# Optimization experiments

Measured on AMD Instinct MI355X. Metric: run time of the kernel, lower is better.

Reference implementation:

```python
import jax, jax.numpy as jnp
import numpy as np

N, M, B = 1024, 8192, 8192  # W: [N, M], x: [B, N]
BLOCK = 32


def activation_quant(x):
    # per-tensor symmetric int8 fake-quant with STE
    scale = 127.0 / jnp.clip(jnp.max(jnp.abs(x)), 1e-8, None)
    x_q = jnp.clip(jnp.round(x * scale), -128.0, 127.0) / scale
    return x + jax.lax.stop_gradient(x_q - x)


def weight_quant_q2_k(w, block_size=BLOCK):
    # blockwise 2-bit quant with top-2 outliers kept at 4-bit, STE
    shape = w.shape
    wf = w.reshape(-1)
    n = wf.shape[0]
    pad = (-n) % block_size
    wf = jnp.pad(wf, (0, pad))
    blocks = wf.reshape(-1, block_size)
    scales = jnp.clip(jnp.max(jnp.abs(blocks), axis=1, keepdims=True), 1e-8, None)
    nb = blocks / scales
    k = min(2, block_size)
    _, top_idx = jax.lax.top_k(jnp.abs(nb), k)
    rows = jnp.arange(nb.shape[0])[:, None]
    top_mask = jnp.zeros(nb.shape, dtype=bool).at[rows, top_idx].set(True)
    q4 = jnp.round(nb * 7.0) / 7.0
    abs_nb = jnp.abs(nb)
    q2 = jnp.sign(nb) * jnp.where(abs_nb > 0.66, 1.0, 1.0 / 3.0)
    q = jnp.where(top_mask, q4, q2) * scales
    w_q = q.reshape(-1)[:n].reshape(shape)
    return w + jax.lax.stop_gradient(w_q - w)


def setup_inputs() -> dict:
    key = jax.random.key(0)
    k1, k2, k3 = jax.random.split(key, 3)
    x = jax.random.normal(k1, (B, N), dtype=jnp.float32)
    W = jax.random.normal(k2, (N, M), dtype=jnp.float32) / np.float32(np.sqrt(M))
    b = jax.random.normal(k3, (N,), dtype=jnp.float32)
    idx = jnp.arange(M // 2, dtype=jnp.int32)            # expanded (quantized) columns
    idx_comp = jnp.arange(M // 2, M, dtype=jnp.int32)    # continuous columns
    return {"x": x, "W": W, "b": b, "idx": idx, "idx_comp": idx_comp}


def reference(x, W, b, idx, idx_comp):
    W_exp_q = weight_quant_q2_k(jnp.take(W, idx, axis=1))   # [N, M/2]
    W_cont = jnp.take(W, idx_comp, axis=1)                  # [N, M/2]
    hidden_exp = activation_quant(x) @ W_exp_q              # [B, M/2]
    hidden_cont = x @ W_cont                                # [B, M/2]
    hidden = (jnp.zeros((x.shape[0], M), dtype=x.dtype)
              .at[:, idx].set(hidden_exp)
              .at[:, idx_comp].set(hidden_cont))            # scatter back to [B, M]
    h_exp = activation_quant(hidden[:, idx])
    out = jax.nn.relu(h_exp @ W_exp_q.T + hidden[:, idx_comp] @ W_cont.T + b)
    return out
```

## Files before the change

kernel.cpp:

```cpp
#include <hip/hip_runtime.h>
#include <hip/hip_bf16.h>
#include <cstdint>


using bf16x8 = __attribute__((ext_vector_type(8))) __bf16;
using f32x4  = __attribute__((ext_vector_type(4))) float;

typedef const __attribute__((address_space(1))) void g_void;
typedef __attribute__((address_space(3))) void l_void;

__device__ __forceinline__ void gload16(const void* g, void* l) {
  __builtin_amdgcn_global_load_lds((g_void*)g, (l_void*)l, 16, 0, 0);
}

__device__ __forceinline__ ushort f2bf(float f) {
  union { float f; unsigned u; } c; c.f = f;
  unsigned r = c.u + 0x7FFFu + ((c.u >> 16) & 1u);
  return (ushort)(r >> 16);
}
__device__ __forceinline__ float bf2f(ushort u) {
  union { unsigned u; float f; } c; c.u = ((unsigned)u) << 16;
  return c.f;
}

__global__ void prep_wa_kernel(const float* __restrict__ W,
                               const float4* __restrict__ x,
                               ushort* __restrict__ Wq,
                               ushort* __restrict__ Wcb,
                               unsigned* __restrict__ amax_bits) {
  const int bidx = blockIdx.x;
  const int tid = threadIdx.x;

  if (bidx < 16384) {
    const int lane = tid & 63;
    const int wave = tid >> 6;
    const int e = lane & 31;
    const int half = lane >> 5;
    const int qb = bidx * 8 + wave * 2 + half;
    const int row = qb >> 7;
    const int m0 = (qb & 127) * 32;
    const float w = W[(size_t)row * 8192 + m0 + e];
    float aw = fabsf(w);
    float m = aw;
    #pragma unroll
    for (int d = 1; d <= 16; d <<= 1) m = fmaxf(m, __shfl_xor(m, d));
    int idx = (aw == m) ? e : 32;
    #pragma unroll
    for (int d = 1; d <= 16; d <<= 1) idx = min(idx, __shfl_xor(idx, d));
    const int i1 = idx;
    float a2 = (e == i1) ? -1.f : aw;
    float m2 = a2;
    #pragma unroll
    for (int d = 1; d <= 16; d <<= 1) m2 = fmaxf(m2, __shfl_xor(m2, d));
    int idx2 = (a2 == m2) ? e : 32;
    #pragma unroll
    for (int d = 1; d <= 16; d <<= 1) idx2 = min(idx2, __shfl_xor(idx2, d));
    const int i2 = idx2;

    const float scale = fmaxf(m, 1e-8f);
    const float nb = w / scale;
    float q;
    if (e == i1 || e == i2) {
      q = rintf(nb * 7.f) / 7.f;
    } else {
      float s = (nb > 0.f) ? 1.f : ((nb < 0.f) ? -1.f : 0.f);
      q = s * ((fabsf(nb) > 0.66f) ? 1.f : (1.f / 3.f));
    }
    Wq[(size_t)row * 4096 + m0 + e] = f2bf(q * scale);
  } else if (bidx < 20480) {
    const int u = (bidx - 16384) * 256 + tid;
    const int row = u >> 10;
    const int c4 = u & 1023;
    float4 v = *(const float4*)(W + (size_t)row * 8192 + 4096 + c4 * 4);
    ushort4 o;
    o.x = f2bf(v.x); o.y = f2bf(v.y); o.z = f2bf(v.z); o.w = f2bf(v.w);
    *(ushort4*)(Wcb + (size_t)row * 4096 + c4 * 4) = o;
  } else {
    float m = 0.f;
    const int base = (bidx - 20480) * 256 + tid;
    const int stride = 2048 * 256;
    for (int i = base; i < 8192 * 1024 / 4; i += stride) {
      float4 v = x[i];
      m = fmaxf(m, fmaxf(fmaxf(fabsf(v.x), fabsf(v.y)),
                         fmaxf(fabsf(v.z), fabsf(v.w))));
    }
    #pragma unroll
    for (int off = 32; off > 0; off >>= 1) m = fmaxf(m, __shfl_down(m, off));
    __shared__ float wm[4];
    int lane = tid & 63, wave = tid >> 6;
    if (lane == 0) wm[wave] = m;
    __syncthreads();
    if (tid == 0) {
      float r = fmaxf(fmaxf(wm[0], wm[1]), fmaxf(wm[2], wm[3]));
      atomicMax(amax_bits, __float_as_uint(r));
    }
  }
}

__global__ void prep_xt_kernel(const ushort* __restrict__ Wq,
                               ushort* __restrict__ WqT,
                               const float4* __restrict__ x,
                               const unsigned* __restrict__ amax_bits,
                               uint4* __restrict__ xq, uint4* __restrict__ xbf) {
  const int bidx = blockIdx.x;
  const int tid = threadIdx.x;

  if (bidx < 1024) {
    __shared__ ushort tile[64][68];
    const int ct = bidx & 63;
    const int rt = bidx >> 6;
    const int col0 = ct * 64, row0 = rt * 64;
    #pragma unroll
    for (int it = 0; it < 4; ++it) {
      const int r = (tid >> 4) + it * 16;
      const int c4 = (tid & 15) * 4;
      *(ushort4*)&tile[r][c4] =
          *(const ushort4*)(Wq + (size_t)(row0 + r) * 4096 + col0 + c4);
    }
    __syncthreads();
    #pragma unroll
    for (int it = 0; it < 4; ++it) {
      const int c = tid >> 2;
      const int rc = (tid & 3) + it * 4;
      ushort4 o;
      o.x = tile[rc * 4 + 0][c];
      o.y = tile[rc * 4 + 1][c];
      o.z = tile[rc * 4 + 2][c];
      o.w = tile[rc * 4 + 3][c];
      *(ushort4*)(WqT + (size_t)(col0 + c) * 1024 + row0 + rc * 4) = o;
    }
  } else {
    const float amax = fmaxf(__uint_as_float(*amax_bits), 1e-8f);
    const float scale = 127.f / amax;
    const int base = (bidx - 1024) * 256 + tid;
    const int stride = 2048 * 256;
    const int n8 = 8192 * 1024 / 8;
    for (int i = base; i < n8; i += stride) {
      float4 a = x[i * 2], b = x[i * 2 + 1];
      float v[8] = {a.x, a.y, a.z, a.w, b.x, b.y, b.z, b.w};
      unsigned qw[4], bw[4];
      #pragma unroll
      for (int j = 0; j < 4; ++j) {
        float q0 = fminf(fmaxf(rintf(v[2 * j] * scale), -128.f), 127.f) / scale;
        float q1 = fminf(fmaxf(rintf(v[2 * j + 1] * scale), -128.f), 127.f) / scale;
        qw[j] = (unsigned)f2bf(q0) | ((unsigned)f2bf(q1) << 16);
        bw[j] = (unsigned)f2bf(v[2 * j]) | ((unsigned)f2bf(v[2 * j + 1]) << 16);
      }
      xq[i] = make_uint4(qw[0], qw[1], qw[2], qw[3]);
      xbf[i] = make_uint4(bw[0], bw[1], bw[2], bw[3]);
    }
  }
}

__global__ __launch_bounds__(256, 2) void gemm1_kernel(
    const ushort* __restrict__ Wcb,
    ushort* __restrict__ G,
    const ushort* __restrict__ Aq, const ushort* __restrict__ BT,
    ushort* __restrict__ Hexp, unsigned* __restrict__ amax_bits) {
  __shared__ __align__(16) ushort As[2][128 * 32];
  __shared__ __align__(16) ushort Bs[2][128 * 32];
  __shared__ float wredmax[4];

  const int bidx = blockIdx.x;
  const int tid = threadIdx.x;
  const int lane = tid & 63, wave = tid >> 6;
  const int l15 = lane & 15, quad = lane >> 4;

  if (bidx < 256) {
    const int gy = bidx >> 4, gx = bidx & 15;
    const int i0 = gy * 64, j0 = gx * 64;
    const int wm2 = (wave >> 1) << 5, wn2 = (wave & 1) << 5;

    const ushort* Ag = Wcb + (size_t)(i0 + (tid >> 2)) * 4096 + (tid & 3) * 8;
    const ushort* Bg = Wcb + (size_t)(j0 + (tid >> 2)) * 4096 + (tid & 3) * 8;
    ushort* Asl = (ushort*)As;
    ushort* Bsl = (ushort*)Bs;

    f32x4 acc[2][2];
    #pragma unroll
    for (int i = 0; i < 2; ++i)
      #pragma unroll
      for (int j = 0; j < 2; ++j) acc[i][j] = (f32x4){0.f, 0.f, 0.f, 0.f};

    for (int k0 = 0; k0 < 4096; k0 += 64) {
      __syncthreads();
      gload16(Ag + k0, Asl + tid * 8);
      gload16(Bg + k0, Bsl + tid * 8);
      gload16(Ag + k0 + 32, Asl + 2048 + tid * 8);
      gload16(Bg + k0 + 32, Bsl + 2048 + tid * 8);
      __syncthreads();
      #pragma unroll
      for (int p = 0; p < 2; ++p) {
        bf16x8 af[2], bfr[2];
        #pragma unroll
        for (int i = 0; i < 2; ++i)
          af[i] = *(const bf16x8*)&Asl[p * 2048 + (wm2 + i * 16 + l15) * 32 + quad * 8];
        #pragma unroll
        for (int j = 0; j < 2; ++j)
          bfr[j] = *(const bf16x8*)&Bsl[p * 2048 + (wn2 + j * 16 + l15) * 32 + quad * 8];
        #pragma unroll
        for (int i = 0; i < 2; ++i)
          #pragma unroll
          for (int j = 0; j < 2; ++j)
            acc[i][j] = __builtin_amdgcn_mfma_f32_16x16x32_bf16(af[i], bfr[j], acc[i][j], 0, 0, 0);
      }
    }
    const int row0 = i0 + wm2 + quad * 4;
    const int col0 = j0 + wn2 + l15;
    #pragma unroll
    for (int i = 0; i < 2; ++i)
      #pragma unroll
      for (int j = 0; j < 2; ++j)
        #pragma unroll
        for (int r = 0; r < 4; ++r)
          G[(size_t)(row0 + i * 16 + r) * 1024 + (col0 + j * 16)] = f2bf(acc[i][j][r]);
    return;
  }

  const int l = bidx - 256;
  const int xcd = l & 7;
  const int s = l >> 3;
  const int t = (xcd << 2) | (s >> 6);
  const int u = s & 63;
  const int bx = ((t & 3) << 3) | (u & 7);
  const int by = ((t >> 2) << 3) | (u >> 3);

  const int wm = (wave >> 1) << 6, wn = (wave & 1) << 6;

  const ushort* Ag = Aq + (size_t)(by * 128 + (tid >> 2)) * 1024 + (tid & 3) * 8;
  const ushort* Bg = BT + (size_t)(bx * 128 + (tid >> 2)) * 1024 + (tid & 3) * 8;
  ushort* Asl0 = As[0] + tid * 8; ushort* Asl1 = As[1] + tid * 8;
  ushort* Bsl0 = Bs[0] + tid * 8; ushort* Bsl1 = Bs[1] + tid * 8;

  f32x4 acc[4][4];
  #pragma unroll
  for (int i = 0; i < 4; ++i)
    #pragma unroll
    for (int j = 0; j < 4; ++j) acc[i][j] = (f32x4){0.f, 0.f, 0.f, 0.f};

  for (int k0 = 0; k0 < 1024; k0 += 64) {
    __syncthreads();
    gload16(Ag + k0, Asl0);
    gload16(Ag + 64 * 1024 + k0, Asl0 + 64 * 32);
    gload16(Bg + k0, Bsl0);
    gload16(Bg + 64 * 1024 + k0, Bsl0 + 64 * 32);
    gload16(Ag + k0 + 32, Asl1);
    gload16(Ag + 64 * 1024 + k0 + 32, Asl1 + 64 * 32);
    gload16(Bg + k0 + 32, Bsl1);
    gload16(Bg + 64 * 1024 + k0 + 32, Bsl1 + 64 * 32);
    __syncthreads();

    #pragma unroll
    for (int p = 0; p < 2; ++p) {
      bf16x8 af[4], bfr[4];
      #pragma unroll
      for (int i = 0; i < 4; ++i)
        af[i] = *(const bf16x8*)&As[p][(wm + i * 16 + l15) * 32 + quad * 8];
      #pragma unroll
      for (int j = 0; j < 4; ++j)
        bfr[j] = *(const bf16x8*)&Bs[p][(wn + j * 16 + l15) * 32 + quad * 8];
      #pragma unroll
      for (int i = 0; i < 4; ++i)
        #pragma unroll
        for (int j = 0; j < 4; ++j)
          acc[i][j] = __builtin_amdgcn_mfma_f32_16x16x32_bf16(af[i], bfr[j], acc[i][j], 0, 0, 0);
    }
  }

  const int row0 = by * 128 + wm + quad * 4;
  const int col0 = bx * 128 + wn + l15;
  float lmax = 0.f;
  #pragma unroll
  for (int i = 0; i < 4; ++i)
    #pragma unroll
    for (int j = 0; j < 4; ++j)
      #pragma unroll
      for (int r = 0; r < 4; ++r) {
        float v = acc[i][j][r];
        lmax = fmaxf(lmax, fabsf(v));
        Hexp[(size_t)(row0 + i * 16 + r) * 4096 + (col0 + j * 16)] = f2bf(v);
      }

  #pragma unroll
  for (int off = 32; off > 0; off >>= 1)
    lmax = fmaxf(lmax, __shfl_down(lmax, off));
  if (lane == 0) wredmax[wave] = lmax;
  __syncthreads();
  if (tid == 0) {
    float m = fmaxf(fmaxf(wredmax[0], wredmax[1]), fmaxf(wredmax[2], wredmax[3]));
    atomicMax(amax_bits, __float_as_uint(m));
  }
}

__global__ void quant_h_kernel(ushort* __restrict__ H,
                               const unsigned* __restrict__ amax_bits) {
  const float amax = fmaxf(__uint_as_float(*amax_bits), 1e-8f);
  const float scale = 127.f / amax;
  const int n8 = 8192 * 4096 / 8;
  for (int i = blockIdx.x * blockDim.x + threadIdx.x; i < n8;
       i += gridDim.x * blockDim.x) {
    uint4* p = (uint4*)H + i;
    uint4 a = *p;
    unsigned w[4] = {a.x, a.y, a.z, a.w};
    #pragma unroll
    for (int j = 0; j < 4; ++j) {
      float lo = bf2f((ushort)(w[j] & 0xFFFF));
      float hi = bf2f((ushort)(w[j] >> 16));
      lo = fminf(fmaxf(rintf(lo * scale), -128.f), 127.f) / scale;
      hi = fminf(fmaxf(rintf(hi * scale), -128.f), 127.f) / scale;
      w[j] = (unsigned)f2bf(lo) | ((unsigned)f2bf(hi) << 16);
    }
    *p = make_uint4(w[0], w[1], w[2], w[3]);
  }
}

__global__ __launch_bounds__(256, 2) void gemm2_kernel(
    const ushort* __restrict__ Hq, const ushort* __restrict__ Wq,
    const ushort* __restrict__ Xb, const ushort* __restrict__ G,
    const float* __restrict__ bias, float* __restrict__ out) {
  __shared__ __align__(16) ushort As[2][128 * 32];
  __shared__ __align__(16) ushort Bs[2][128 * 32];

  const int l = blockIdx.x;
  const int xcd = l & 7;
  const int s = l >> 3;
  const int by = (xcd << 3) | (s >> 3);
  const int bx = s & 7;

  const int tid = threadIdx.x;
  const int lane = tid & 63, wave = tid >> 6;
  const int wm = (wave >> 1) << 6, wn = (wave & 1) << 6;
  const int l15 = lane & 15, quad = lane >> 4;

  ushort* Asl0 = As[0] + tid * 8; ushort* Asl1 = As[1] + tid * 8;
  ushort* Bsl0 = Bs[0] + tid * 8; ushort* Bsl1 = Bs[1] + tid * 8;

  f32x4 acc[4][4];
  #pragma unroll
  for (int i = 0; i < 4; ++i)
    #pragma unroll
    for (int j = 0; j < 4; ++j) acc[i][j] = (f32x4){0.f, 0.f, 0.f, 0.f};

  {
    const ushort* Ag = Hq + (size_t)(by * 128 + (tid >> 2)) * 4096 + (tid & 3) * 8;
    const ushort* Bg = Wq + (size_t)(bx * 128 + (tid >> 2)) * 4096 + (tid & 3) * 8;
    for (int k0 = 0; k0 < 4096; k0 += 64) {
      __syncthreads();
      gload16(Ag + k0, Asl0);
      gload16(Ag + (size_t)64 * 4096 + k0, Asl0 + 64 * 32);
      gload16(Bg + k0, Bsl0);
      gload16(Bg + (size_t)64 * 4096 + k0, Bsl0 + 64 * 32);
      gload16(Ag + k0 + 32, Asl1);
      gload16(Ag + (size_t)64 * 4096 + k0 + 32, Asl1 + 64 * 32);
      gload16(Bg + k0 + 32, Bsl1);
      gload16(Bg + (size_t)64 * 4096 + k0 + 32, Bsl1 + 64 * 32);
      __syncthreads();
      #pragma unroll
      for (int p = 0; p < 2; ++p) {
        bf16x8 af[4], bfr[4];
        #pragma unroll
        for (int i = 0; i < 4; ++i)
          af[i] = *(const bf16x8*)&As[p][(wm + i * 16 + l15) * 32 + quad * 8];
        #pragma unroll
        for (int j = 0; j < 4; ++j)
          bfr[j] = *(const bf16x8*)&Bs[p][(wn + j * 16 + l15) * 32 + quad * 8];
        #pragma unroll
        for (int i = 0; i < 4; ++i)
          #pragma unroll
          for (int j = 0; j < 4; ++j)
            acc[i][j] = __builtin_amdgcn_mfma_f32_16x16x32_bf16(af[i], bfr[j], acc[i][j], 0, 0, 0);
      }
    }
  }
  {
    const ushort* Ag = Xb + (size_t)(by * 128 + (tid >> 2)) * 1024 + (tid & 3) * 8;
    const ushort* Bg = G + (size_t)(bx * 128 + (tid >> 2)) * 1024 + (tid & 3) * 8;
    for (int k0 = 0; k0 < 1024; k0 += 64) {
      __syncthreads();
      gload16(Ag + k0, Asl0);
      gload16(Ag + 64 * 1024 + k0, Asl0 + 64 * 32);
      gload16(Bg + k0, Bsl0);
      gload16(Bg + 64 * 1024 + k0, Bsl0 + 64 * 32);
      gload16(Ag + k0 + 32, Asl1);
      gload16(Ag + 64 * 1024 + k0 + 32, Asl1 + 64 * 32);
      gload16(Bg + k0 + 32, Bsl1);
      gload16(Bg + 64 * 1024 + k0 + 32, Bsl1 + 64 * 32);
      __syncthreads();
      #pragma unroll
      for (int p = 0; p < 2; ++p) {
        bf16x8 af[4], bfr[4];
        #pragma unroll
        for (int i = 0; i < 4; ++i)
          af[i] = *(const bf16x8*)&As[p][(wm + i * 16 + l15) * 32 + quad * 8];
        #pragma unroll
        for (int j = 0; j < 4; ++j)
          bfr[j] = *(const bf16x8*)&Bs[p][(wn + j * 16 + l15) * 32 + quad * 8];
        #pragma unroll
        for (int i = 0; i < 4; ++i)
          #pragma unroll
          for (int j = 0; j < 4; ++j)
            acc[i][j] = __builtin_amdgcn_mfma_f32_16x16x32_bf16(af[i], bfr[j], acc[i][j], 0, 0, 0);
      }
    }
  }

  const int row0 = by * 128 + wm + quad * 4;
  const int col0 = bx * 128 + wn + l15;
  #pragma unroll
  for (int i = 0; i < 4; ++i)
    #pragma unroll
    for (int j = 0; j < 4; ++j) {
      float bv = bias[col0 + j * 16];
      #pragma unroll
      for (int r = 0; r < 4; ++r) {
        float v = acc[i][j][r] + bv;
        v = fmaxf(v, 0.f);
        out[(size_t)(row0 + i * 16 + r) * 1024 + (col0 + j * 16)] = v;
      }
    }
}

extern "C" void kernel_launch(void* const* d_in, const int* in_sizes, int n_in,
                              void* d_out, int out_size, void* d_ws, size_t ws_size,
                              hipStream_t stream) {
  (void)in_sizes; (void)n_in; (void)out_size; (void)ws_size;
  const float* x = (const float*)d_in[0];
  const float* W = (const float*)d_in[1];
  const float* b = (const float*)d_in[2];

  char* ws = (char*)d_ws;
  unsigned* scal = (unsigned*)ws;
  ushort* xq   = (ushort*)(ws + 256);
  ushort* xbf  = xq   + (size_t)8192 * 1024;
  ushort* Wq   = xbf  + (size_t)8192 * 1024;
  ushort* WqT  = Wq   + (size_t)1024 * 4096;
  ushort* Wcb  = WqT  + (size_t)4096 * 1024;
  ushort* G    = Wcb  + (size_t)1024 * 4096;
  ushort* Hexp = G    + (size_t)1024 * 1024;

  hipMemsetAsync(scal, 0, 256, stream);
  prep_wa_kernel<<<22528, 256, 0, stream>>>(W, (const float4*)x, Wq, Wcb, scal);
  prep_xt_kernel<<<3072, 256, 0, stream>>>(Wq, WqT, (const float4*)x, scal,
                                           (uint4*)xq, (uint4*)xbf);
  gemm1_kernel<<<2304, 256, 0, stream>>>(Wcb, G, xq, WqT, Hexp, scal + 1);
  quant_h_kernel<<<2048, 256, 0, stream>>>(Hexp, scal + 1);
  gemm2_kernel<<<512, 256, 0, stream>>>(Hexp, Wq, xbf, G, b, (float*)d_out);
}
```

Baseline: 358.3 us.

## Fuse weight transpose into quantization and enlarge Gram GEMM tiles

Writes the transposed quantized weight directly from the quantization pass via an LDS tile, removing a separate transpose pass that re-read Wq. The Gram GEMM on the continuous weights now uses 128x128 tiles (64 blocks) instead of 64x64 (256 blocks), improving reuse but making fewer, longer blocks that may form a tail. The quant_h launch grid is also doubled.

```diff
diff --git a/kernel.cpp b/kernel.cpp
--- a/kernel.cpp
+++ b/kernel.cpp
@@ -26,49 +26,64 @@
 __global__ void prep_wa_kernel(const float* __restrict__ W,
                                const float4* __restrict__ x,
                                ushort* __restrict__ Wq,
+                               ushort* __restrict__ WqT,
                                ushort* __restrict__ Wcb,
                                unsigned* __restrict__ amax_bits) {
   const int bidx = blockIdx.x;
   const int tid = threadIdx.x;
 
-  if (bidx < 16384) {
-    const int lane = tid & 63;
-    const int wave = tid >> 6;
-    const int e = lane & 31;
-    const int half = lane >> 5;
-    const int qb = bidx * 8 + wave * 2 + half;
-    const int row = qb >> 7;
-    const int m0 = (qb & 127) * 32;
-    const float w = W[(size_t)row * 8192 + m0 + e];
-    float aw = fabsf(w);
-    float m = aw;
-    #pragma unroll
-    for (int d = 1; d <= 16; d <<= 1) m = fmaxf(m, __shfl_xor(m, d));
-    int idx = (aw == m) ? e : 32;
-    #pragma unroll
-    for (int d = 1; d <= 16; d <<= 1) idx = min(idx, __shfl_xor(idx, d));
-    const int i1 = idx;
-    float a2 = (e == i1) ? -1.f : aw;
-    float m2 = a2;
-    #pragma unroll
-    for (int d = 1; d <= 16; d <<= 1) m2 = fmaxf(m2, __shfl_xor(m2, d));
-    int idx2 = (a2 == m2) ? e : 32;
-    #pragma unroll
-    for (int d = 1; d <= 16; d <<= 1) idx2 = min(idx2, __shfl_xor(idx2, d));
-    const int i2 = idx2;
-
-    const float scale = fmaxf(m, 1e-8f);
-    const float nb = w / scale;
-    float q;
-    if (e == i1 || e == i2) {
-      q = rintf(nb * 7.f) / 7.f;
-    } else {
-      float s = (nb > 0.f) ? 1.f : ((nb < 0.f) ? -1.f : 0.f);
-      q = s * ((fabsf(nb) > 0.66f) ? 1.f : (1.f / 3.f));
-    }
-    Wq[(size_t)row * 4096 + m0 + e] = f2bf(q * scale);
-  } else if (bidx < 20480) {
-    const int u = (bidx - 16384) * 256 + tid;
+  if (bidx < 1024) {
+    __shared__ __align__(16) ushort tile[64][72];
+    const int rt = bidx >> 6;
+    const int ct = bidx & 63;
+    const int r0 = rt * 64, c0 = ct * 64;
+    const int e = tid & 31;
+    const int hw = tid >> 5;
+    #pragma unroll
+    for (int it = 0; it < 16; ++it) {
+      const int g = it * 8 + hw;
+      const int row = g >> 1;
+      const int cg = (g & 1) * 32;
+      const float w = W[(size_t)(r0 + row) * 8192 + c0 + cg + e];
+      float aw = fabsf(w);
+      float m = aw;
+      #pragma unroll
+      for (int d = 1; d <= 16; d <<= 1) m = fmaxf(m, __shfl_xor(m, d));
+      int idx = (aw == m) ? e : 32;
+      #pragma unroll
+      for (int d = 1; d <= 16; d <<= 1) idx = min(idx, __shfl_xor(idx, d));
+      const int i1 = idx;
+      float a2 = (e == i1) ? -1.f : aw;
+      float m2 = a2;
+      #pragma unroll
+      for (int d = 1; d <= 16; d <<= 1) m2 = fmaxf(m2, __shfl_xor(m2, d));
+      int idx2 = (a2 == m2) ? e : 32;
+      #pragma unroll
+      for (int d = 1; d <= 16; d <<= 1) idx2 = min(idx2, __shfl_xor(idx2, d));
+      const int i2 = idx2;
+
+      const float scale = fmaxf(m, 1e-8f);
+      const float nb = w / scale;
+      float q;
+      if (e == i1 || e == i2) {
+        q = rintf(nb * 7.f) / 7.f;
+      } else {
+        float s = (nb > 0.f) ? 1.f : ((nb < 0.f) ? -1.f : 0.f);
+        q = s * ((fabsf(nb) > 0.66f) ? 1.f : (1.f / 3.f));
+      }
+      const ushort qb = f2bf(q * scale);
+      Wq[(size_t)(r0 + row) * 4096 + c0 + cg + e] = qb;
+      tile[cg + e][row] = qb;
+    }
+    __syncthreads();
+    const int c = tid >> 2;
+    const int q4 = (tid & 3) * 16;
+    uint4 v0 = *(const uint4*)&tile[c][q4];
+    uint4 v1 = *(const uint4*)&tile[c][q4 + 8];
+    *(uint4*)(WqT + (size_t)(c0 + c) * 1024 + r0 + q4) = v0;
+    *(uint4*)(WqT + (size_t)(c0 + c) * 1024 + r0 + q4 + 8) = v1;
+  } else if (bidx < 5120) {
+    const int u = (bidx - 1024) * 256 + tid;
     const int row = u >> 10;
     const int c4 = u & 1023;
     float4 v = *(const float4*)(W + (size_t)row * 8192 + 4096 + c4 * 4);
@@ -77,7 +92,7 @@
     *(ushort4*)(Wcb + (size_t)row * 4096 + c4 * 4) = o;
   } else {
     float m = 0.f;
-    const int base = (bidx - 20480) * 256 + tid;
+    const int base = (bidx - 5120) * 256 + tid;
     const int stride = 2048 * 256;
     for (int i = base; i < 8192 * 1024 / 4; i += stride) {
       float4 v = x[i];
@@ -97,58 +112,27 @@
   }
 }
 
-__global__ void prep_xt_kernel(const ushort* __restrict__ Wq,
-                               ushort* __restrict__ WqT,
-                               const float4* __restrict__ x,
-                               const unsigned* __restrict__ amax_bits,
-                               uint4* __restrict__ xq, uint4* __restrict__ xbf) {
-  const int bidx = blockIdx.x;
-  const int tid = threadIdx.x;
-
-  if (bidx < 1024) {
-    __shared__ ushort tile[64][68];
-    const int ct = bidx & 63;
-    const int rt = bidx >> 6;
-    const int col0 = ct * 64, row0 = rt * 64;
-    #pragma unroll
-    for (int it = 0; it < 4; ++it) {
-      const int r = (tid >> 4) + it * 16;
-      const int c4 = (tid & 15) * 4;
-      *(ushort4*)&tile[r][c4] =
-          *(const ushort4*)(Wq + (size_t)(row0 + r) * 4096 + col0 + c4);
-    }
-    __syncthreads();
-    #pragma unroll
-    for (int it = 0; it < 4; ++it) {
-      const int c = tid >> 2;
-      const int rc = (tid & 3) + it * 4;
-      ushort4 o;
-      o.x = tile[rc * 4 + 0][c];
-      o.y = tile[rc * 4 + 1][c];
-      o.z = tile[rc * 4 + 2][c];
-      o.w = tile[rc * 4 + 3][c];
-      *(ushort4*)(WqT + (size_t)(col0 + c) * 1024 + row0 + rc * 4) = o;
-    }
-  } else {
-    const float amax = fmaxf(__uint_as_float(*amax_bits), 1e-8f);
-    const float scale = 127.f / amax;
-    const int base = (bidx - 1024) * 256 + tid;
-    const int stride = 2048 * 256;
-    const int n8 = 8192 * 1024 / 8;
-    for (int i = base; i < n8; i += stride) {
-      float4 a = x[i * 2], b = x[i * 2 + 1];
-      float v[8] = {a.x, a.y, a.z, a.w, b.x, b.y, b.z, b.w};
-      unsigned qw[4], bw[4];
-      #pragma unroll
-      for (int j = 0; j < 4; ++j) {
-        float q0 = fminf(fmaxf(rintf(v[2 * j] * scale), -128.f), 127.f) / scale;
-        float q1 = fminf(fmaxf(rintf(v[2 * j + 1] * scale), -128.f), 127.f) / scale;
-        qw[j] = (unsigned)f2bf(q0) | ((unsigned)f2bf(q1) << 16);
-        bw[j] = (unsigned)f2bf(v[2 * j]) | ((unsigned)f2bf(v[2 * j + 1]) << 16);
-      }
-      xq[i] = make_uint4(qw[0], qw[1], qw[2], qw[3]);
-      xbf[i] = make_uint4(bw[0], bw[1], bw[2], bw[3]);
-    }
+__global__ void prep_x_kernel(const float4* __restrict__ x,
+                              const unsigned* __restrict__ amax_bits,
+                              uint4* __restrict__ xq, uint4* __restrict__ xbf) {
+  const float amax = fmaxf(__uint_as_float(*amax_bits), 1e-8f);
+  const float scale = 127.f / amax;
+  const int base = blockIdx.x * 256 + threadIdx.x;
+  const int stride = 2048 * 256;
+  const int n8 = 8192 * 1024 / 8;
+  for (int i = base; i < n8; i += stride) {
+    float4 a = x[i * 2], b = x[i * 2 + 1];
+    float v[8] = {a.x, a.y, a.z, a.w, b.x, b.y, b.z, b.w};
+    unsigned qw[4], bw[4];
+    #pragma unroll
+    for (int j = 0; j < 4; ++j) {
+      float q0 = fminf(fmaxf(rintf(v[2 * j] * scale), -128.f), 127.f) / scale;
+      float q1 = fminf(fmaxf(rintf(v[2 * j + 1] * scale), -128.f), 127.f) / scale;
+      qw[j] = (unsigned)f2bf(q0) | ((unsigned)f2bf(q1) << 16);
+      bw[j] = (unsigned)f2bf(v[2 * j]) | ((unsigned)f2bf(v[2 * j + 1]) << 16);
+    }
+    xq[i] = make_uint4(qw[0], qw[1], qw[2], qw[3]);
+    xbf[i] = make_uint4(bw[0], bw[1], bw[2], bw[3]);
   }
 }
 
@@ -165,59 +149,62 @@
   const int tid = threadIdx.x;
   const int lane = tid & 63, wave = tid >> 6;
   const int l15 = lane & 15, quad = lane >> 4;
-
-  if (bidx < 256) {
-    const int gy = bidx >> 4, gx = bidx & 15;
-    const int i0 = gy * 64, j0 = gx * 64;
-    const int wm2 = (wave >> 1) << 5, wn2 = (wave & 1) << 5;
-
+  const int wm = (wave >> 1) << 6, wn = (wave & 1) << 6;
+
+  ushort* Asl0 = As[0] + tid * 8; ushort* Asl1 = As[1] + tid * 8;
+  ushort* Bsl0 = Bs[0] + tid * 8; ushort* Bsl1 = Bs[1] + tid * 8;
+
+  f32x4 acc[4][4];
+  #pragma unroll
+  for (int i = 0; i < 4; ++i)
+    #pragma unroll
+    for (int j = 0; j < 4; ++j) acc[i][j] = (f32x4){0.f, 0.f, 0.f, 0.f};
+
+  if (bidx < 64) {
+    const int gy = bidx >> 3, gx = bidx & 7;
+    const int i0 = gy * 128, j0 = gx * 128;
     const ushort* Ag = Wcb + (size_t)(i0 + (tid >> 2)) * 4096 + (tid & 3) * 8;
     const ushort* Bg = Wcb + (size_t)(j0 + (tid >> 2)) * 4096 + (tid & 3) * 8;
-    ushort* Asl = (ushort*)As;
-    ushort* Bsl = (ushort*)Bs;
-
-    f32x4 acc[2][2];
-    #pragma unroll
-    for (int i = 0; i < 2; ++i)
-      #pragma unroll
-      for (int j = 0; j < 2; ++j) acc[i][j] = (f32x4){0.f, 0.f, 0.f, 0.f};
-
     for (int k0 = 0; k0 < 4096; k0 += 64) {
       __syncthreads();
-      gload16(Ag + k0, Asl + tid * 8);
-      gload16(Bg + k0, Bsl + tid * 8);
-      gload16(Ag + k0 + 32, Asl + 2048 + tid * 8);
-      gload16(Bg + k0 + 32, Bsl + 2048 + tid * 8);
+      gload16(Ag + k0, Asl0);
+      gload16(Ag + (size_t)64 * 4096 + k0, Asl0 + 64 * 32);
+      gload16(Bg + k0, Bsl0);
+      gload16(Bg + (size_t)64 * 4096 + k0, Bsl0 + 64 * 32);
+      gload16(Ag + k0 + 32, Asl1);
+      gload16(Ag + (size_t)64 * 4096 + k0 + 32, Asl1 + 64 * 32);
+      gload16(Bg + k0 + 32, Bsl1);
+      gload16(Bg + (size_t)64 * 4096 + k0 + 32, Bsl1 + 64 * 32);
       __syncthreads();
       #pragma unroll
       for (int p = 0; p < 2; ++p) {
-        bf16x8 af[2], bfr[2];
-        #pragma unroll
-        for (int i = 0; i < 2; ++i)
-          af[i] = *(const bf16x8*)&Asl[p * 2048 + (wm2 + i * 16 + l15) * 32 + quad * 8];
-        #pragma unroll
-        for (int j = 0; j < 2; ++j)
-          bfr[j] = *(const bf16x8*)&Bsl[p * 2048 + (wn2 + j * 16 + l15) * 32 + quad * 8];
-        #pragma unroll
-        for (int i = 0; i < 2; ++i)
+        bf16x8 af[4], bfr[4];
+        #pragma unroll
+        for (int i = 0; i < 4; ++i)
+          af[i] = *(const bf16x8*)&As[p][(wm + i * 16 + l15) * 32 + quad * 8];
+        #pragma unroll
+        for (int j = 0; j < 4; ++j)
+          bfr[j] = *(const bf16x8*)&Bs[p][(wn + j * 16 + l15) * 32 + quad * 8];
+        #pragma unroll
+        for (int i = 0; i < 4; ++i)
           #pragma unroll
-          for (int j = 0; j < 2; ++j)
+          for (int j = 0; j < 4; ++j)
             acc[i][j] = __builtin_amdgcn_mfma_f32_16x16x32_bf16(af[i], bfr[j], acc[i][j], 0, 0, 0);
       }
     }
-    const int row0 = i0 + wm2 + quad * 4;
-    const int col0 = j0 + wn2 + l15;
-    #pragma unroll
-    for (int i = 0; i < 2; ++i)
-      #pragma unroll
-      for (int j = 0; j < 2; ++j)
+    const int row0 = i0 + wm + quad * 4;
+    const int col0 = j0 + wn + l15;
+    #pragma unroll
+    for (int i = 0; i < 4; ++i)
+      #pragma unroll
+      for (int j = 0; j < 4; ++j)
         #pragma unroll
         for (int r = 0; r < 4; ++r)
           G[(size_t)(row0 + i * 16 + r) * 1024 + (col0 + j * 16)] = f2bf(acc[i][j][r]);
     return;
   }
 
-  const int l = bidx - 256;
+  const int l = bidx - 64;
   const int xcd = l & 7;
   const int s = l >> 3;
   const int t = (xcd << 2) | (s >> 6);
@@ -225,18 +212,8 @@
   const int bx = ((t & 3) << 3) | (u & 7);
   const int by = ((t >> 2) << 3) | (u >> 3);
 
-  const int wm = (wave >> 1) << 6, wn = (wave & 1) << 6;
-
   const ushort* Ag = Aq + (size_t)(by * 128 + (tid >> 2)) * 1024 + (tid & 3) * 8;
   const ushort* Bg = BT + (size_t)(bx * 128 + (tid >> 2)) * 1024 + (tid & 3) * 8;
-  ushort* Asl0 = As[0] + tid * 8; ushort* Asl1 = As[1] + tid * 8;
-  ushort* Bsl0 = Bs[0] + tid * 8; ushort* Bsl1 = Bs[1] + tid * 8;
-
-  f32x4 acc[4][4];
-  #pragma unroll
-  for (int i = 0; i < 4; ++i)
-    #pragma unroll
-    for (int j = 0; j < 4; ++j) acc[i][j] = (f32x4){0.f, 0.f, 0.f, 0.f};
 
   for (int k0 = 0; k0 < 1024; k0 += 64) {
     __syncthreads();
@@ -439,10 +416,10 @@
   ushort* Hexp = G    + (size_t)1024 * 1024;
 
   hipMemsetAsync(scal, 0, 256, stream);
-  prep_wa_kernel<<<22528, 256, 0, stream>>>(W, (const float4*)x, Wq, Wcb, scal);
-  prep_xt_kernel<<<3072, 256, 0, stream>>>(Wq, WqT, (const float4*)x, scal,
-                                           (uint4*)xq, (uint4*)xbf);
-  gemm1_kernel<<<2304, 256, 0, stream>>>(Wcb, G, xq, WqT, Hexp, scal + 1);
-  quant_h_kernel<<<2048, 256, 0, stream>>>(Hexp, scal + 1);
+  prep_wa_kernel<<<7168, 256, 0, stream>>>(W, (const float4*)x, Wq, WqT, Wcb, scal);
+  prep_x_kernel<<<2048, 256, 0, stream>>>((const float4*)x, scal,
+                                          (uint4*)xq, (uint4*)xbf);
+  gemm1_kernel<<<2112, 256, 0, stream>>>(Wcb, G, xq, WqT, Hexp, scal + 1);
+  quant_h_kernel<<<4096, 256, 0, stream>>>(Hexp, scal + 1);
   gemm2_kernel<<<512, 256, 0, stream>>>(Hexp, Wq, xbf, G, b, (float*)d_out);
 }
```

Result: faster. 344.3 us (-3.9%).
